# Optimization experiments

Measured on AMD Instinct MI355X. Metric: run time of the kernel, lower is better.

## Reference

```python
import jax, jax.numpy as jnp
import numpy as np

B, L, D = 4, 4096, 256
INIT_ALPHA = -2.0
INV_TEMP = 1.0 / 0.1


def setup_inputs() -> dict:
    key = jax.random.key(0)
    k1, k2, k3, k4 = jax.random.split(key, 4)
    latents = jax.random.normal(k1, (B, L, D), dtype=jnp.float32)
    current_coords = jax.random.normal(k2, (B, L, 2), dtype=jnp.float32)
    # Linear(D, D, bias=False) weights (torch stores [out, in]; y = x @ W.T)
    lim = 1.0 / np.sqrt(D)
    Wq = jax.random.uniform(k3, (D, D), minval=-lim, maxval=lim, dtype=jnp.float32)
    Wk = jax.random.uniform(k4, (D, D), minval=-lim, maxval=lim, dtype=jnp.float32)
    alpha_raw = jnp.asarray(INIT_ALPHA, dtype=jnp.float32)
    return {"latents": latents, "current_coords": current_coords,
            "Wq": Wq, "Wk": Wk, "alpha_raw": alpha_raw, "layer_idx": 3}


def _l2norm(x, eps=1e-12):
    # F.normalize(dim=-1): x / max(||x||, eps)
    n = jnp.sqrt(jnp.sum(x * x, axis=-1, keepdims=True))
    return x / jnp.maximum(n, eps)


def reference(latents, current_coords, Wq, Wk, alpha_raw, layer_idx):
    # pred_idx selection (share_weights=True): 0 if layer_idx==0 else 1;
    # layer_idx=3 -> params given are for pred_idx=1.
    q = _l2norm(jnp.einsum('bld,ed->ble', latents, Wq))  # [B,L,D]
    k = _l2norm(jnp.einsum('bld,ed->ble', latents, Wk))  # [B,L,D]
    scores = jnp.einsum('bld,bmd->blm', q, k) * INV_TEMP  # [B,L,L]
    scores = jnp.clip(scores, -50.0, 50.0)
    W = jax.nn.softmax(scores, axis=-1)                   # [B,L,L]
    alpha = jax.nn.sigmoid(alpha_raw)
    # M = alpha*W + (1-alpha)*I; M @ coords == alpha*(W@coords) + (1-alpha)*coords
    new_coords = alpha * jnp.einsum('blm,bmc->blc', W, current_coords) \
                 + (1.0 - alpha) * current_coords
    displacement = new_coords - current_coords
    return (new_coords, displacement)
```

## Files before the change

### kernel.cpp

```cpp
#include <hip/hip_runtime.h>
#include <hip/hip_bf16.h>

#define BB 4
#define LL 4096
#define DD 256
#define MM (BB * LL)
#define NSPLIT 8
#define BM 256
#define NQB (LL / BM)
#define KPS (LL / NSPLIT)
#define KT 64
#define NKT (KPS / KT)

typedef short short8 __attribute__((ext_vector_type(8)));
typedef float floatx4 __attribute__((ext_vector_type(4)));

#define SCALE_LOG2E 14.426950408889634f

__device__ __forceinline__ unsigned short f2bf(float f) {
    __hip_bfloat16 h = __float2bfloat16(f);
    union { __hip_bfloat16 h; unsigned short s; } c; c.h = h; return c.s;
}

__device__ __forceinline__ float fast_exp2(float x) {
#if __has_builtin(__builtin_amdgcn_exp2f)
    return __builtin_amdgcn_exp2f(x);
#else
    return exp2f(x);
#endif
}

__device__ __forceinline__ void pinv(short8& v) {
    asm volatile("" : "+v"(v));
}

__device__ __forceinline__ void stage16(const char* g, char* l, int lane) {
#if __has_builtin(__builtin_amdgcn_global_load_lds)
    __builtin_amdgcn_global_load_lds(
        (const __attribute__((address_space(1))) void*)(g + lane * 16),
        (__attribute__((address_space(3))) void*)l, 16, 0, 0);
#else
    *(short8*)(l + lane * 16) = *(const short8*)(g + lane * 16);
#endif
}

__global__ __launch_bounds__(256) void cvt_swz_kernel(
    const float* __restrict__ srcq, const float* __restrict__ srck,
    unsigned short* __restrict__ dstq, unsigned short* __restrict__ dstk)
{
    const int which = blockIdx.x >> 5;
    const float* src = which ? srck : srcq;
    unsigned short* dst = which ? dstk : dstq;
    const int t = (blockIdx.x & 31) * 256 + threadIdx.x;
    const int r = t >> 5, c = t & 31;
    const float4 v0 = ((const float4*)src)[t * 2];
    const float4 v1 = ((const float4*)src)[t * 2 + 1];
    short8 o;
    o[0] = (short)f2bf(v0.x); o[1] = (short)f2bf(v0.y);
    o[2] = (short)f2bf(v0.z); o[3] = (short)f2bf(v0.w);
    o[4] = (short)f2bf(v1.x); o[5] = (short)f2bf(v1.y);
    o[6] = (short)f2bf(v1.z); o[7] = (short)f2bf(v1.w);
    const int cs = c ^ (r & 7);
    *(short8*)(dst + (size_t)r * DD + cs * 8) = o;
}

__global__ __launch_bounds__(256) void proj_norm_kernel(
    const float* __restrict__ latents,
    const __hip_bfloat16* __restrict__ Wq,
    const __hip_bfloat16* __restrict__ Wk,
    __hip_bfloat16* __restrict__ qn,
    __hip_bfloat16* __restrict__ kn)
{
    __shared__ char lds[65536];

    const int tid  = threadIdx.x;
    const int wave = tid >> 6;
    const int lane = tid & 63;
    const int n15  = lane & 15;
    const int quad = lane >> 4;
    const int sw   = n15 & 7;

    const int pass  = blockIdx.x & 1;
    const int rbase = (blockIdx.x >> 1) * 64;
    const int m0    = rbase + wave * 16;
    const int r160  = rbase >> 4;

    short8 afrag[8];
    const float* Abase = latents + (size_t)(m0 + n15) * DD + quad * 8;
#pragma unroll
    for (int kk = 0; kk < 8; ++kk) {
        const float4 v0 = *(const float4*)(Abase + kk * 32);
        const float4 v1 = *(const float4*)(Abase + kk * 32 + 4);
        short8 f;
        f[0] = (short)f2bf(v0.x); f[1] = (short)f2bf(v0.y);
        f[2] = (short)f2bf(v0.z); f[3] = (short)f2bf(v0.w);
        f[4] = (short)f2bf(v1.x); f[5] = (short)f2bf(v1.y);
        f[6] = (short)f2bf(v1.z); f[7] = (short)f2bf(v1.w);
        afrag[kk] = f;
    }

    const char* W = (const char*)(pass ? Wk : Wq);

    floatx4 acc[16];
#pragma unroll
    for (int ct = 0; ct < 16; ++ct) acc[ct] = (floatx4){0.f, 0.f, 0.f, 0.f};

    {
        const char* src = W + wave * 8192;
        char* dst = lds + wave * 8192;
#pragma unroll
        for (int j = 0; j < 8; ++j) stage16(src + j * 1024, dst + j * 1024, lane);
    }

    for (int round = 0; round < 4; ++round) {
        __syncthreads();
        if (round + 1 < 4) {
            const char* src = W + (size_t)(round + 1) * 32768 + wave * 8192;
            char* dst = lds + ((round + 1) & 1) * 32768 + wave * 8192;
#pragma unroll
            for (int j = 0; j < 8; ++j) stage16(src + j * 1024, dst + j * 1024, lane);
        }
        const char* buf = lds + (round & 1) * 32768;
#pragma unroll
        for (int jt = 0; jt < 4; ++jt) {
            const int ct = round * 4 + jt;
            const char* lbase = buf + (jt * 16 + n15) * 512;
            floatx4 a = acc[ct];
            __builtin_amdgcn_s_setprio(1);
#pragma unroll
            for (int kk = 0; kk < 8; ++kk) {
                const int chunk = (4 * kk + quad) ^ sw;
                short8 bfr = *(const short8*)(lbase + chunk * 16);
                a = __builtin_amdgcn_mfma_f32_16x16x32_bf16(afrag[kk], bfr, a, 0, 0, 0);
            }
            __builtin_amdgcn_s_setprio(0);
            acc[ct] = a;
        }
    }

    float ss[4] = {0.f, 0.f, 0.f, 0.f};
#pragma unroll
    for (int ct = 0; ct < 16; ++ct)
#pragma unroll
        for (int r = 0; r < 4; ++r) ss[r] += acc[ct][r] * acc[ct][r];
#pragma unroll
    for (int r = 0; r < 4; ++r) {
        ss[r] += __shfl_xor(ss[r], 1, 64);
        ss[r] += __shfl_xor(ss[r], 2, 64);
        ss[r] += __shfl_xor(ss[r], 4, 64);
        ss[r] += __shfl_xor(ss[r], 8, 64);
    }
    float sc[4];
#pragma unroll
    for (int r = 0; r < 4; ++r) {
        sc[r] = 1.f / fmaxf(sqrtf(ss[r]), 1e-12f);
        if (pass == 0) sc[r] *= SCALE_LOG2E;
    }

    unsigned short* tb = (unsigned short*)lds;
#pragma unroll
    for (int h = 0; h < 2; ++h) {
        __syncthreads();
#pragma unroll
        for (int cth = 0; cth < 8; ++cth) {
            const int ct = h * 8 + cth;
            const int col = cth * 16 + n15;
#pragma unroll
            for (int r = 0; r < 4; ++r) {
                const int rl = wave * 16 + quad * 4 + r;
                tb[rl * 136 + col] = f2bf(acc[ct][r] * sc[r]);
            }
        }
        __syncthreads();
        if (pass == 0) {
#pragma unroll
            for (int j = 0; j < 4; ++j) {
                const int g = tid + j * 256;
                const int n15r = g & 15, q2 = (g >> 4) & 3, kkh = (g >> 6) & 3, r16l = (g >> 8) & 3;
                const int rl = r16l * 16 + n15r;
                short8 v = *(const short8*)(tb + rl * 136 + kkh * 32 + q2 * 8);
                const size_t chunk = (((size_t)(r160 + r16l) * 8 + (h * 4 + kkh)) * 4 + q2) * 16 + n15r;
                *(short8*)((char*)qn + chunk * 16) = v;
            }
        } else {
#pragma unroll
            for (int j = 0; j < 4; ++j) {
                const int g = tid + j * 256;
                const int csl = g & 15, rl = g >> 4;
                const int row = rbase + rl;
                const int ci = csl ^ (row & 7);
                short8 v = *(const short8*)(tb + rl * 136 + ci * 8);
                *(short8*)((char*)kn + (size_t)row * 512 + (h * 16 + csl) * 16) = v;
            }
        }
    }
}

__global__ __launch_bounds__(256, 2) void attn_kernel(
    const __hip_bfloat16* __restrict__ qn,
    const __hip_bfloat16* __restrict__ kn,
    const float* __restrict__ coords,
    float* __restrict__ partials)
{
    __shared__ char lds[2 * 32768 + 4096];
    char* clds = lds + 2 * 32768;

    const int tid  = threadIdx.x;
    const int wave = tid >> 6;
    const int lane = tid & 63;
    const int n15  = lane & 15;
    const int quad = lane >> 4;
    const int sw   = n15 & 7;

    int bs = (blockIdx.x & 7) * 64 + (blockIdx.x >> 3);
    const int qb    = bs % NQB;    bs /= NQB;
    const int split = bs % NSPLIT; bs /= NSPLIT;
    const int b     = bs;

    const int mw = b * LL + qb * BM + wave * 64;

    const int key_base = b * LL + split * KPS;
    const char* ksrc = (const char*)kn + (size_t)key_base * 512;

    stage16((const char*)coords + (size_t)key_base * 8 + wave * 1024,
            clds + wave * 1024, lane);
    asm volatile("" ::: "memory");

    short8 aq[4][8];
    const int t16 = mw >> 4;
#pragma unroll
    for (int rt = 0; rt < 4; ++rt)
#pragma unroll
        for (int kk = 0; kk < 8; ++kk) {
            const size_t chunk = (((size_t)(t16 + rt) * 8 + kk) * 4 + quad) * 16 + n15;
            aq[rt][kk] = *(const short8*)((const char*)qn + chunk * 16);
        }
#pragma unroll
    for (int rt = 0; rt < 4; ++rt)
#pragma unroll
        for (int kk = 0; kk < 8; ++kk) pinv(aq[rt][kk]);
    asm volatile("" ::: "memory");

#pragma unroll
    for (int t = 0; t < 2; ++t) {
        const char* src = ksrc + (size_t)t * KT * 512 + wave * 8192;
        char* dst = lds + t * 32768 + wave * 8192;
#pragma unroll
        for (int j = 0; j < 8; ++j) stage16(src + j * 1024, dst + j * 1024, lane);
        asm volatile("" ::: "memory");
    }

    float s0[4][4], s1[4][4], s2[4][4];
#pragma unroll
    for (int rt = 0; rt < 4; ++rt)
#pragma unroll
        for (int r = 0; r < 4; ++r) { s0[rt][r] = 0.f; s1[rt][r] = 0.f; s2[rt][r] = 0.f; }

#pragma unroll
    for (int kt = 0; kt < NKT; ++kt) {
        if (kt == NKT - 1) asm volatile("s_waitcnt vmcnt(0)" ::: "memory");
        else               asm volatile("s_waitcnt vmcnt(8)" ::: "memory");
        __builtin_amdgcn_s_barrier();

        const char* buf = lds + (kt & 1) * 32768;

#pragma unroll
        for (int ct = 0; ct < 4; ++ct) {
            const float2 cc = *(const float2*)(clds + (kt * KT + ct * 16 + n15) * 8);

            floatx4 acc[4];
#pragma unroll
            for (int rt = 0; rt < 4; ++rt) acc[rt] = (floatx4){0.f, 0.f, 0.f, 0.f};
            const char* lbase = buf + (ct * 16 + n15) * 512;

            __builtin_amdgcn_s_setprio(1);
#pragma unroll
            for (int kk = 0; kk < 8; ++kk) {
                const int chunk = (4 * kk + quad) ^ sw;
                const short8 bfr = *(const short8*)(lbase + chunk * 16);
#pragma unroll
                for (int rt = 0; rt < 4; ++rt)
                    acc[rt] = __builtin_amdgcn_mfma_f32_16x16x32_bf16(aq[rt][kk], bfr, acc[rt], 0, 0, 0);
            }
            __builtin_amdgcn_s_setprio(0);

#pragma unroll
            for (int rt = 0; rt < 4; ++rt)
#pragma unroll
                for (int r = 0; r < 4; ++r) {
                    const float e = fast_exp2(acc[rt][r]);
                    s0[rt][r] += e;
                    s1[rt][r] = fmaf(cc.x, e, s1[rt][r]);
                    s2[rt][r] = fmaf(cc.y, e, s2[rt][r]);
                }
        }

        if (kt + 2 < NKT) {
            __builtin_amdgcn_s_barrier();
            const char* src = ksrc + (size_t)(kt + 2) * KT * 512 + wave * 8192;
            char* dst = lds + (kt & 1) * 32768 + wave * 8192;
#pragma unroll
            for (int j = 0; j < 8; ++j) stage16(src + j * 1024, dst + j * 1024, lane);
            asm volatile("" ::: "memory");
        }
    }

#pragma unroll
    for (int rt = 0; rt < 4; ++rt)
#pragma unroll
        for (int r = 0; r < 4; ++r)
#pragma unroll
            for (int mask = 1; mask <= 8; mask <<= 1) {
                s0[rt][r] += __shfl_xor(s0[rt][r], mask, 64);
                s1[rt][r] += __shfl_xor(s1[rt][r], mask, 64);
                s2[rt][r] += __shfl_xor(s2[rt][r], mask, 64);
            }

    if (n15 == 0) {
#pragma unroll
        for (int rt = 0; rt < 4; ++rt)
#pragma unroll
            for (int r = 0; r < 4; ++r) {
                const int m = mw + rt * 16 + quad * 4 + r;
                float* p = partials + ((size_t)split * MM + m) * 4;
                p[0] = s0[rt][r];
                p[1] = s1[rt][r];
                p[2] = s2[rt][r];
            }
    }
}

__global__ __launch_bounds__(256) void finish_kernel(
    const float* __restrict__ partials,
    const float* __restrict__ coords,
    const float* __restrict__ alpha_raw,
    float* __restrict__ out)
{
    const int m = blockIdx.x * 256 + threadIdx.x;

    const float alpha = 1.f / (1.f + __expf(-alpha_raw[0]));

    float s0 = 0.f, s1 = 0.f, s2 = 0.f;
#pragma unroll
    for (int s = 0; s < NSPLIT; ++s) {
        const float4 v = *(const float4*)(partials + ((size_t)s * MM + m) * 4);
        s0 += v.x; s1 += v.y; s2 += v.z;
    }

    const float cx = coords[m * 2];
    const float cy = coords[m * 2 + 1];
    const float inv = 1.f / s0;
    const float nx = alpha * (s1 * inv) + (1.f - alpha) * cx;
    const float ny = alpha * (s2 * inv) + (1.f - alpha) * cy;

    out[m * 2]     = nx;
    out[m * 2 + 1] = ny;
    out[2 * MM + m * 2]     = nx - cx;
    out[2 * MM + m * 2 + 1] = ny - cy;
}

extern "C" void kernel_launch(void* const* d_in, const int* in_sizes, int n_in,
                              void* d_out, int out_size, void* d_ws, size_t ws_size,
                              hipStream_t stream) {
    const float* latents   = (const float*)d_in[0];
    const float* coords    = (const float*)d_in[1];
    const float* Wq        = (const float*)d_in[2];
    const float* Wk        = (const float*)d_in[3];
    const float* alpha_raw = (const float*)d_in[4];

    char* ws = (char*)d_ws;
    __hip_bfloat16* qn   = (__hip_bfloat16*)ws;
    __hip_bfloat16* kn   = (__hip_bfloat16*)(ws + (size_t)8 * 1024 * 1024);
    __hip_bfloat16* wq_b = (__hip_bfloat16*)(ws + (size_t)16 * 1024 * 1024);
    __hip_bfloat16* wk_b = (__hip_bfloat16*)(ws + (size_t)16 * 1024 * 1024 + 131072);
    float* partials      = (float*)(ws + (size_t)16 * 1024 * 1024 + 262144);

    float* out = (float*)d_out;

    cvt_swz_kernel<<<64, 256, 0, stream>>>(Wq, Wk, (unsigned short*)wq_b, (unsigned short*)wk_b);
    proj_norm_kernel<<<512, 256, 0, stream>>>(latents, wq_b, wk_b, qn, kn);
    attn_kernel<<<BB * NQB * NSPLIT, 256, 0, stream>>>(qn, kn, coords, partials);
    finish_kernel<<<MM / 256, 256, 0, stream>>>(partials, coords, alpha_raw, out);
}
```

Measured before the change: 124.6 us.

## Compute softmax-weighted coordinate sums with a second MFMA instead of scalar FMAs

The per-element exp, sum and coordinate FMA accumulation is replaced by writing bf16 probabilities to LDS and running a second bf16 MFMA against a value fragment of [x, y, 1]. Each coordinate is split into high and low bf16 parts to keep precision. The key tile is halved so the probability buffer fits in LDS, and the final 16-lane shuffle reduction is cut down to two shuffles. The aim is to move VALU work onto the matrix units, at the cost of an extra barrier per tile, LDS round-trips and bf16 rounding of the probabilities.

```diff
diff --git a/kernel.cpp b/kernel.cpp
--- a/kernel.cpp
+++ b/kernel.cpp
@@ -9,7 +9,7 @@
 #define BM 256
 #define NQB (LL / BM)
 #define KPS (LL / NSPLIT)
-#define KT 64
+#define KT 32
 #define NKT (KPS / KT)
 
 typedef short short8 __attribute__((ext_vector_type(8)));
@@ -20,6 +20,17 @@
 __device__ __forceinline__ unsigned short f2bf(float f) {
     __hip_bfloat16 h = __float2bfloat16(f);
     union { __hip_bfloat16 h; unsigned short s; } c; c.h = h; return c.s;
+}
+
+__device__ __forceinline__ float bf2f(unsigned short s) {
+    union { unsigned short s; __hip_bfloat16 h; } c; c.s = s;
+    return __bfloat162float(c.h);
+}
+
+__device__ __forceinline__ unsigned int pk2bf(float lo, float hi) {
+    union { __hip_bfloat162 h2; unsigned int u; } c;
+    c.h2 = __float22bfloat162_rn(float2{lo, hi});
+    return c.u;
 }
 
 __device__ __forceinline__ float fast_exp2(float x) {
@@ -202,8 +213,7 @@
     const float* __restrict__ coords,
     float* __restrict__ partials)
 {
-    __shared__ char lds[2 * 32768 + 4096];
-    char* clds = lds + 2 * 32768;
+    __shared__ char lds[2 * 16384 + 4 * 8192 + 4096];
 
     const int tid  = threadIdx.x;
     const int wave = tid >> 6;
@@ -212,13 +222,15 @@
     const int quad = lane >> 4;
     const int sw   = n15 & 7;
 
+    char* plds = lds + 32768 + wave * 8192;
+    char* clds = lds + 65536;
+
     int bs = (blockIdx.x & 7) * 64 + (blockIdx.x >> 3);
     const int qb    = bs % NQB;    bs /= NQB;
     const int split = bs % NSPLIT; bs /= NSPLIT;
     const int b     = bs;
 
     const int mw = b * LL + qb * BM + wave * 64;
-
     const int key_base = b * LL + split * KPS;
     const char* ksrc = (const char*)kn + (size_t)key_base * 512;
 
@@ -243,31 +255,40 @@
 
 #pragma unroll
     for (int t = 0; t < 2; ++t) {
-        const char* src = ksrc + (size_t)t * KT * 512 + wave * 8192;
-        char* dst = lds + t * 32768 + wave * 8192;
-#pragma unroll
-        for (int j = 0; j < 8; ++j) stage16(src + j * 1024, dst + j * 1024, lane);
+        const char* src = ksrc + (size_t)t * KT * 512 + wave * 4096;
+        char* dst = lds + t * 16384 + wave * 4096;
+#pragma unroll
+        for (int j = 0; j < 4; ++j) stage16(src + j * 1024, dst + j * 1024, lane);
         asm volatile("" ::: "memory");
     }
 
-    float s0[4][4], s1[4][4], s2[4][4];
-#pragma unroll
-    for (int rt = 0; rt < 4; ++rt)
-#pragma unroll
-        for (int r = 0; r < 4; ++r) { s0[rt][r] = 0.f; s1[rt][r] = 0.f; s2[rt][r] = 0.f; }
-
-#pragma unroll
+    floatx4 acc_pv[4];
+#pragma unroll
+    for (int rt = 0; rt < 4; ++rt) acc_pv[rt] = (floatx4){0.f, 0.f, 0.f, 0.f};
+
+    const int vc  = n15 & 3;
+    const int vg  = n15 >> 2;
+
+#pragma unroll 2
     for (int kt = 0; kt < NKT; ++kt) {
         if (kt == NKT - 1) asm volatile("s_waitcnt vmcnt(0)" ::: "memory");
-        else               asm volatile("s_waitcnt vmcnt(8)" ::: "memory");
+        else               asm volatile("s_waitcnt vmcnt(4)" ::: "memory");
         __builtin_amdgcn_s_barrier();
 
-        const char* buf = lds + (kt & 1) * 32768;
-
-#pragma unroll
-        for (int ct = 0; ct < 4; ++ct) {
-            const float2 cc = *(const float2*)(clds + (kt * KT + ct * 16 + n15) * 8);
-
+        const char* buf = lds + (kt & 1) * 16384;
+
+        short8 vfrag;
+#pragma unroll
+        for (int j = 0; j < 8; ++j) {
+            const float2 xy = *(const float2*)(clds + (size_t)(kt * KT + quad * 8 + j) * 8);
+            const float raw = (vc == 0) ? xy.x : (vc == 1) ? xy.y : (vc == 2 ? 1.f : 0.f);
+            const unsigned short hb = f2bf(raw);
+            const unsigned short lb = f2bf(raw - bf2f(hb));
+            vfrag[j] = (short)((vg == 0) ? hb : (vg == 1 ? lb : (unsigned short)0));
+        }
+
+#pragma unroll
+        for (int ct = 0; ct < 2; ++ct) {
             floatx4 acc[4];
 #pragma unroll
             for (int rt = 0; rt < 4; ++rt) acc[rt] = (floatx4){0.f, 0.f, 0.f, 0.f};
@@ -280,53 +301,55 @@
                 const short8 bfr = *(const short8*)(lbase + chunk * 16);
 #pragma unroll
                 for (int rt = 0; rt < 4; ++rt)
-                    acc[rt] = __builtin_amdgcn_mfma_f32_16x16x32_bf16(aq[rt][kk], bfr, acc[rt], 0, 0, 0);
+                    acc[rt] = __builtin_amdgcn_mfma_f32_16x16x32_bf16(bfr, aq[rt][kk], acc[rt], 0, 0, 0);
             }
             __builtin_amdgcn_s_setprio(0);
 
-#pragma unroll
-            for (int rt = 0; rt < 4; ++rt)
-#pragma unroll
-                for (int r = 0; r < 4; ++r) {
-                    const float e = fast_exp2(acc[rt][r]);
-                    s0[rt][r] += e;
-                    s1[rt][r] = fmaf(cc.x, e, s1[rt][r]);
-                    s2[rt][r] = fmaf(cc.y, e, s2[rt][r]);
-                }
-        }
-
+            const int slot = ct * 2 + (quad >> 1);
+#pragma unroll
+            for (int rt = 0; rt < 4; ++rt) {
+                const float e0 = fast_exp2(acc[rt][0]);
+                const float e1 = fast_exp2(acc[rt][1]);
+                const float e2 = fast_exp2(acc[rt][2]);
+                const float e3 = fast_exp2(acc[rt][3]);
+                const unsigned long long p64 =
+                    (unsigned long long)pk2bf(e0, e1) |
+                    ((unsigned long long)pk2bf(e2, e3) << 32);
+                *(unsigned long long*)(plds + rt * 2048 + n15 * 128 +
+                                       ((slot ^ sw) << 4) + ((quad & 1) << 3)) = p64;
+            }
+        }
+
+        __builtin_amdgcn_s_barrier();
         if (kt + 2 < NKT) {
-            __builtin_amdgcn_s_barrier();
-            const char* src = ksrc + (size_t)(kt + 2) * KT * 512 + wave * 8192;
-            char* dst = lds + (kt & 1) * 32768 + wave * 8192;
-#pragma unroll
-            for (int j = 0; j < 8; ++j) stage16(src + j * 1024, dst + j * 1024, lane);
+            const char* src = ksrc + (size_t)(kt + 2) * KT * 512 + wave * 4096;
+            char* dst = lds + (kt & 1) * 16384 + wave * 4096;
+#pragma unroll
+            for (int j = 0; j < 4; ++j) stage16(src + j * 1024, dst + j * 1024, lane);
             asm volatile("" ::: "memory");
         }
-    }
-
-#pragma unroll
-    for (int rt = 0; rt < 4; ++rt)
-#pragma unroll
-        for (int r = 0; r < 4; ++r)
-#pragma unroll
-            for (int mask = 1; mask <= 8; mask <<= 1) {
-                s0[rt][r] += __shfl_xor(s0[rt][r], mask, 64);
-                s1[rt][r] += __shfl_xor(s1[rt][r], mask, 64);
-                s2[rt][r] += __shfl_xor(s2[rt][r], mask, 64);
-            }
-
-    if (n15 == 0) {
-#pragma unroll
-        for (int rt = 0; rt < 4; ++rt)
-#pragma unroll
-            for (int r = 0; r < 4; ++r) {
-                const int m = mw + rt * 16 + quad * 4 + r;
-                float* p = partials + ((size_t)split * MM + m) * 4;
-                p[0] = s0[rt][r];
-                p[1] = s1[rt][r];
-                p[2] = s2[rt][r];
-            }
+
+#pragma unroll
+        for (int rt = 0; rt < 4; ++rt) {
+            const short8 pfrag = *(const short8*)(plds + rt * 2048 + n15 * 128 +
+                                                  ((quad ^ sw) << 4));
+            acc_pv[rt] = __builtin_amdgcn_mfma_f32_16x16x32_bf16(vfrag, pfrag, acc_pv[rt], 0, 0, 0);
+        }
+    }
+
+#pragma unroll
+    for (int rt = 0; rt < 4; ++rt) {
+        float t0 = acc_pv[rt][0], t1 = acc_pv[rt][1], t2 = acc_pv[rt][2];
+        t0 += __shfl_xor(t0, 16, 64); t0 += __shfl_xor(t0, 32, 64);
+        t1 += __shfl_xor(t1, 16, 64); t1 += __shfl_xor(t1, 32, 64);
+        t2 += __shfl_xor(t2, 16, 64); t2 += __shfl_xor(t2, 32, 64);
+        if (lane < 16) {
+            const int m = mw + rt * 16 + n15;
+            float* p = partials + ((size_t)split * MM + m) * 4;
+            p[0] = t2;
+            p[1] = t0;
+            p[2] = t1;
+        }
     }
 }
 
```

After: 132.0 us. +5.9%, slower.
